# Optimization experiments

Hardware: AMD Instinct MI355X
Metric: run time of the kernel (lower is better)

## Reference

```python
import jax, jax.numpy as jnp
import numpy as np

FEA, DK, H = 512, 64, 8
B, L = 4, 2048
EPS = 1e-5


def _layernorm(x, g, b):
    mu = jnp.mean(x, axis=-1, keepdims=True)
    var = jnp.mean(jnp.square(x - mu), axis=-1, keepdims=True)
    return (x - mu) * jax.lax.rsqrt(var + EPS) * g + b


def setup_inputs() -> dict:
    key = jax.random.key(0)
    ks = jax.random.split(key, 12)
    d = {
        'qx': jax.random.normal(ks[0], (B, L, FEA), jnp.float32),
        'kx': jax.random.normal(ks[1], (B, L, FEA), jnp.float32),
        'vx': jax.random.normal(ks[2], (B, L, FEA), jnp.float32),
        'maskPAD': jax.random.randint(ks[3], (B, L, L), 0, 2, jnp.int32),
        # attention projections (stored as [in, out]); biases zero-init as in module
        'wq': jax.random.normal(ks[4], (FEA, DK * H), jnp.float32) * 0.02,
        'bq': jnp.zeros((DK * H,), jnp.float32),
        'wk': jax.random.normal(ks[5], (FEA, DK * H), jnp.float32) * 0.02,
        'bk': jnp.zeros((DK * H,), jnp.float32),
        'wv': jax.random.normal(ks[6], (FEA, DK * H), jnp.float32) * 0.02,
        'bv': jnp.zeros((DK * H,), jnp.float32),
        'wo': jax.random.normal(ks[7], (DK * H, FEA), jnp.float32) * 0.02,
        'bo': jnp.zeros((FEA,), jnp.float32),
        # FFN
        'w1': jax.random.normal(ks[8], (FEA, 4 * FEA), jnp.float32) * 0.02,
        'b1': jnp.zeros((4 * FEA,), jnp.float32),
        'w2': jax.random.normal(ks[9], (4 * FEA, FEA), jnp.float32) * 0.02,
        'b2': jnp.zeros((FEA,), jnp.float32),
        # layer norms
        'ln1_g': jnp.ones((FEA,), jnp.float32),
        'ln1_b': jnp.zeros((FEA,), jnp.float32),
        'ln2_g': jnp.ones((FEA,), jnp.float32),
        'ln2_b': jnp.zeros((FEA,), jnp.float32),
    }
    return d


def reference(qx, kx, vx, maskPAD, wq, bq, wk, bk, wv, bv, wo, bo,
              w1, b1, w2, b2, ln1_g, ln1_b, ln2_g, ln2_b):
    b, l, _ = qx.shape
    # project and split heads: [B, H, L, DK]
    q = (qx @ wq + bq).reshape(b, l, H, DK).transpose(0, 2, 1, 3)
    k = (kx @ wk + bk).reshape(b, l, H, DK).transpose(0, 2, 1, 3)
    v = (vx @ wv + bv).reshape(b, l, H, DK).transpose(0, 2, 1, 3)
    scores = jnp.einsum('bhqd,bhkd->bhqk', q, k) / np.sqrt(DK)  # [B,H,L,L]
    mask = (maskPAD == 0)[:, None, :, :]
    scores = jnp.where(mask, jnp.float32(-2 ** 15 + 1), scores)
    alpha = jax.nn.softmax(scores, axis=-1)
    z = jnp.einsum('bhqk,bhkd->bhqd', alpha, v)  # [B,H,L,DK]
    z = z.transpose(0, 2, 1, 3).reshape(b, l, H * DK)
    z = z @ wo + bo
    # post-LN FFN block (dropout = identity at inference)
    zn = _layernorm(vx + z, ln1_g, ln1_b)
    ffn = jax.nn.gelu(zn @ w1 + b1, approximate=False) @ w2 + b2
    return _layernorm(zn + ffn, ln2_g, ln2_b)
```

## Files before the change

### kernel.cpp

```cpp
#include <hip/hip_runtime.h>
#include <cstdint>


typedef __bf16 bf16;
typedef __bf16 bf16x8 __attribute__((ext_vector_type(8)));
typedef __bf16 bf16x2 __attribute__((ext_vector_type(2)));
typedef float floatx4 __attribute__((ext_vector_type(4)));
typedef unsigned uint2v __attribute__((ext_vector_type(2)));

__device__ __forceinline__ floatx4 mfma_bf16(bf16x8 a, bf16x8 b, floatx4 c) {
  return __builtin_amdgcn_mfma_f32_16x16x32_bf16(a, b, c, 0, 0, 0);
}

__device__ __forceinline__ void load_lds_16(const void* g, void* l) {
  auto gp = reinterpret_cast<const void __attribute__((address_space(1)))*>(
      reinterpret_cast<uintptr_t>(g));
  auto lp = reinterpret_cast<void __attribute__((address_space(3)))*>(
      (unsigned int)reinterpret_cast<uintptr_t>(l));
  __builtin_amdgcn_global_load_lds(gp, lp, 16, 0, 0);
}

__device__ __forceinline__ unsigned pack2(float a, float b) {
  bf16x2 p;
  p[0] = (bf16)a;
  p[1] = (bf16)b;
  return __builtin_bit_cast(unsigned, p);
}

__device__ __forceinline__ float gelu_f(float x) {
  float t = 0.7978845608f * (x + 0.044715f * x * x * x);
  float e = __builtin_amdgcn_exp2f(t * 2.885390082f);
  float th = 1.0f - 2.0f * __builtin_amdgcn_rcpf(e + 1.0f);
  return 0.5f * x * (1.0f + th);
}

#define PLANE128 2064
#define PLANE64 1040
#define KVCH 8320

__global__ void __launch_bounds__(256) prep_k(
    const float* __restrict__ wq, const float* __restrict__ wk,
    const float* __restrict__ wv, const float* __restrict__ wo,
    bf16* __restrict__ wqT, bf16* __restrict__ wkT, bf16* __restrict__ wvT,
    bf16* __restrict__ woT, const float* __restrict__ w1,
    bf16* __restrict__ w1T, const float* __restrict__ w2,
    bf16* __restrict__ w2T, const int* __restrict__ mpad,
    unsigned long long* __restrict__ mbits, const float* __restrict__ qx,
    const float* __restrict__ kx, const float* __restrict__ vx,
    bf16* __restrict__ xb) {
  __shared__ float tile[32][33];
  int bid = blockIdx.x, tid = threadIdx.x;
  int tx = tid & 31, ty = tid >> 5;
  if (bid < 3072) {
    const float* in;
    bf16* out;
    int m0, k0, K, M;
    if (bid < 1024) {
      int z = bid >> 8, r = bid & 255;
      in = (z == 0) ? wq : (z == 1) ? wk : (z == 2) ? wv : wo;
      out = (z == 0) ? wqT : (z == 1) ? wkT : (z == 2) ? wvT : woT;
      m0 = (r & 15) * 32; k0 = (r >> 4) * 32; K = 512; M = 512;
    } else if (bid < 2048) {
      int r = bid - 1024;
      in = w1; out = w1T;
      m0 = (r & 63) * 32; k0 = (r >> 6) * 32; K = 512; M = 2048;
    } else {
      int r = bid - 2048;
      in = w2; out = w2T;
      m0 = (r & 15) * 32; k0 = (r >> 4) * 32; K = 2048; M = 512;
    }
    for (int i = ty; i < 32; i += 8)
      tile[i][tx] = in[(size_t)(k0 + i) * M + m0 + tx];
    __syncthreads();
    for (int i = ty; i < 32; i += 8)
      out[(size_t)(m0 + i) * K + k0 + tx] = (bf16)tile[tx][i];
  } else if (bid < 5120) {
    int r = bid - 3072;
    int w0 = r * 128 + (tid >> 6) * 32;
    int lane = tid & 63;
#pragma unroll 4
    for (int i = 0; i < 32; ++i) {
      int w = w0 + i;
      int v = mpad[(size_t)w * 64 + lane];
      unsigned long long bmask = __ballot(v != 0);
      if (lane == 0) mbits[w] = bmask;
    }
  } else {
    int r = bid - 5120;
    size_t idx = ((size_t)r * 256 + tid) * 8;
    int sel = (int)(idx >> 22);
    size_t off = idx & ((1u << 22) - 1);
    const float* src = (sel == 0) ? qx : (sel == 1) ? kx : vx;
    float4 a = *(const float4*)(src + off);
    float4 b = *(const float4*)(src + off + 4);
    bf16x8 o;
    o[0] = (bf16)a.x; o[1] = (bf16)a.y; o[2] = (bf16)a.z; o[3] = (bf16)a.w;
    o[4] = (bf16)b.x; o[5] = (bf16)b.y; o[6] = (bf16)b.z; o[7] = (bf16)b.w;
    *(bf16x8*)(xb + idx) = o;
  }
}

template <int EPI>
__device__ __forceinline__ void epi_store(void* Cout, int n, int m, int M,
                                          float val) {
  if constexpr (EPI == 3) {
    ((bf16*)Cout)[(size_t)n * M + m] = (bf16)gelu_f(val);
  } else if constexpr (EPI == 4) {
    ((float*)Cout)[(size_t)n * M + m] = val;
  } else {
    ((float*)Cout)[(size_t)n * M + m] += val;
  }
}

template <int EPI, bool TALL>
__global__ void __launch_bounds__(256) gemm_bt(const bf16* __restrict__ A,
                                               const bf16* __restrict__ Bt,
                                               const float* __restrict__ bias,
                                               void* __restrict__ Cout,
                                               int M, int K, int lda, int ldb) {
  __shared__ __attribute__((aligned(16))) char As[8 * PLANE128];
  __shared__ __attribute__((aligned(16))) char Bs[TALL ? 8 * PLANE64 : 8 * PLANE128];
  int tid = threadIdx.x, wave = tid >> 6, lane = tid & 63;
  int lrow = lane & 15, quad = lane >> 4;
  int n0 = blockIdx.y * 128;
  int m0 = blockIdx.x * (TALL ? 64 : 128);
  int wr = wave >> 1, wc = wave & 1;
  floatx4 zero4 = {0.f, 0.f, 0.f, 0.f};
  constexpr int NI = TALL ? 2 : 4;
  floatx4 acc[NI][4];
#pragma unroll
  for (int i = 0; i < NI; ++i)
#pragma unroll
    for (int j = 0; j < 4; ++j) acc[i][j] = zero4;
  for (int k0 = 0; k0 < K; k0 += 64) {
    __syncthreads();
#pragma unroll
    for (int h = 0; h < 2; ++h) {
      int p = wave + 4 * h;
#pragma unroll
      for (int j = 0; j < 2; ++j) {
        int row = j * 64 + lane;
        load_lds_16(A + (size_t)(n0 + row) * lda + k0 + p * 8,
                    As + p * PLANE128 + j * 1024 + lane * 16);
      }
      if constexpr (TALL) {
        load_lds_16(Bt + (size_t)(m0 + lane) * ldb + k0 + p * 8,
                    Bs + p * PLANE64 + lane * 16);
      } else {
#pragma unroll
        for (int j = 0; j < 2; ++j) {
          int row = j * 64 + lane;
          load_lds_16(Bt + (size_t)(m0 + row) * ldb + k0 + p * 8,
                      Bs + p * PLANE128 + j * 1024 + lane * 16);
        }
      }
    }
    __syncthreads();
#pragma unroll
    for (int h = 0; h < 2; ++h) {
      int pb = h * 4 + quad;
      bf16x8 af[NI], bfr[4];
#pragma unroll
      for (int i = 0; i < NI; ++i) {
        int row = (TALL ? wave * 32 : wr * 64) + i * 16 + lrow;
        af[i] = *(const bf16x8*)(As + pb * PLANE128 + row * 16);
      }
#pragma unroll
      for (int j = 0; j < 4; ++j) {
        if constexpr (TALL)
          bfr[j] = *(const bf16x8*)(Bs + pb * PLANE64 + (j * 16 + lrow) * 16);
        else
          bfr[j] = *(const bf16x8*)(Bs + pb * PLANE128 +
                                    (wc * 64 + j * 16 + lrow) * 16);
      }
#pragma unroll
      for (int i = 0; i < NI; ++i)
#pragma unroll
        for (int j = 0; j < 4; ++j)
          acc[i][j] = mfma_bf16(af[i], bfr[j], acc[i][j]);
    }
  }
  float bv[4];
#pragma unroll
  for (int j = 0; j < 4; ++j) {
    int m = m0 + (TALL ? 0 : wc * 64) + j * 16 + lrow;
    bv[j] = (EPI == 5) ? 0.f : bias[m];
  }
#pragma unroll
  for (int i = 0; i < NI; ++i)
#pragma unroll
    for (int j = 0; j < 4; ++j)
#pragma unroll
      for (int r = 0; r < 4; ++r) {
        int n = n0 + (TALL ? wave * 32 : wr * 64) + i * 16 + quad * 4 + r;
        int m = m0 + (TALL ? 0 : wc * 64) + j * 16 + lrow;
        epi_store<EPI>(Cout, n, m, M, acc[i][j][r] + bv[j]);
      }
}

__global__ void __launch_bounds__(256) qkv_k(const bf16* __restrict__ xb,
                                             const bf16* __restrict__ wqT,
                                             const bf16* __restrict__ wkT,
                                             const bf16* __restrict__ wvT,
                                             const float* __restrict__ bq,
                                             const float* __restrict__ bk,
                                             const float* __restrict__ bv_,
                                             bf16* __restrict__ qh,
                                             bf16* __restrict__ kh,
                                             bf16* __restrict__ vt) {
  __shared__ __attribute__((aligned(16))) char As[8 * PLANE128];
  __shared__ __attribute__((aligned(16))) char Bs[8 * PLANE128];
  int tid = threadIdx.x, wave = tid >> 6, lane = tid & 63;
  int lrow = lane & 15, quad = lane >> 4;
  int seg = blockIdx.y >> 6;
  int n0 = (blockIdx.y & 63) * 128, m0 = blockIdx.x * 128;
  const bf16* Af = xb + ((size_t)seg << 22);
  const bf16* Bt = (seg == 0) ? wqT : (seg == 1) ? wkT : wvT;
  const float* bias = (seg == 0) ? bq : (seg == 1) ? bk : bv_;
  bf16* out = (seg == 0) ? qh : (seg == 1) ? kh : vt;
  int wr = wave >> 1, wc = wave & 1;
  floatx4 zero4 = {0.f, 0.f, 0.f, 0.f};
  floatx4 acc[4][4];
#pragma unroll
  for (int i = 0; i < 4; ++i)
#pragma unroll
    for (int j = 0; j < 4; ++j) acc[i][j] = zero4;
  for (int k0 = 0; k0 < 512; k0 += 64) {
    __syncthreads();
#pragma unroll
    for (int h = 0; h < 2; ++h) {
      int p = wave + 4 * h;
#pragma unroll
      for (int j = 0; j < 2; ++j) {
        int row = j * 64 + lane;
        load_lds_16(Af + (size_t)(n0 + row) * 512 + k0 + p * 8,
                    As + p * PLANE128 + j * 1024 + lane * 16);
        load_lds_16(Bt + (size_t)(m0 + row) * 512 + k0 + p * 8,
                    Bs + p * PLANE128 + j * 1024 + lane * 16);
      }
    }
    __syncthreads();
#pragma unroll
    for (int h = 0; h < 2; ++h) {
      int pb = h * 4 + quad;
      bf16x8 af[4], bfr[4];
#pragma unroll
      for (int t = 0; t < 4; ++t) {
        af[t] = *(const bf16x8*)(As + pb * PLANE128 + (wr * 64 + t * 16 + lrow) * 16);
        bfr[t] = *(const bf16x8*)(Bs + pb * PLANE128 + (wc * 64 + t * 16 + lrow) * 16);
      }
#pragma unroll
      for (int i = 0; i < 4; ++i)
#pragma unroll
        for (int j = 0; j < 4; ++j) acc[i][j] = mfma_bf16(af[i], bfr[j], acc[i][j]);
    }
  }
  float bvv[4];
#pragma unroll
  for (int j = 0; j < 4; ++j) bvv[j] = bias[m0 + wc * 64 + j * 16 + lrow];
  const float qscale = 0.1803368801f;
#pragma unroll
  for (int i = 0; i < 4; ++i)
#pragma unroll
    for (int j = 0; j < 4; ++j)
#pragma unroll
      for (int r = 0; r < 4; ++r) {
        int n = n0 + wr * 64 + i * 16 + quad * 4 + r;
        int m = m0 + wc * 64 + j * 16 + lrow;
        float val = acc[i][j][r] + bvv[j];
        int bb = n >> 11, l = n & 2047, hh = m >> 6, d = m & 63;
        if (seg == 0) {
          out[((size_t)((bb * 8 + hh) * 2048 + l)) * 64 + d] =
              (bf16)(val * qscale);
        } else {
          size_t tb_ = ((size_t)((bb * 8 + hh) * 32 + (l >> 6))) * 4096;
          if (seg == 1)
            out[tb_ + (d >> 3) * 512 + (l & 63) * 8 + (d & 7)] = (bf16)val;
          else
            out[tb_ + ((l >> 3) & 7) * 512 + d * 8 + (l & 7)] = (bf16)val;
        }
      }
}

__global__ void __launch_bounds__(512, 4) attn_k(const bf16* __restrict__ Qh,
                                                 const bf16* __restrict__ Kh,
                                                 const bf16* __restrict__ Vt,
                                                 const unsigned long long* __restrict__ MB,
                                                 bf16* __restrict__ Z) {
  __shared__ __attribute__((aligned(16))) char smem[8 * KVCH];
  int qt = blockIdx.x, h = blockIdx.y, b = blockIdx.z;
  int tid = threadIdx.x, wave = tid >> 6, lane = tid & 63;
  int hw = wave >> 2, wl = wave & 3;
  int lrow = lane & 15, quad = lane >> 4;
  int q0 = qt * 128;
  size_t headbase = (size_t)(b * 8 + h) * 2048 * 64;

  bf16x8 qf[2][2];
#pragma unroll
  for (int u = 0; u < 2; ++u) {
    const bf16* Qp =
        Qh + headbase + (size_t)(q0 + wl * 32 + u * 16 + lrow) * 64 + quad * 8;
    qf[u][0] = *(const bf16x8*)Qp;
    qf[u][1] = *(const bf16x8*)(Qp + 32);
  }

  floatx4 zero4 = {0.f, 0.f, 0.f, 0.f};
  floatx4 o_acc[2][4], acc_l[2];
#pragma unroll
  for (int u = 0; u < 2; ++u) {
    acc_l[u] = zero4;
#pragma unroll
    for (int dt = 0; dt < 4; ++dt) o_acc[u][dt] = zero4;
  }
  bf16x8 ones;
#pragma unroll
  for (int j = 0; j < 8; ++j) ones[j] = (bf16)1.0f;

  const bf16* Kt0 = Kh + headbase;
  const bf16* Vt0 = Vt + headbase;
  const uint2* MB0 =
      (const uint2*)(MB + ((size_t)b * 2048 + q0 + wl * 32 + lrow) * 32);
  int sh = quad * 4;

  char* KsH = smem + hw * 2 * KVCH;
  char* VsH = smem + 4 * KVCH + hw * 2 * KVCH;

  auto stage = [&](int buf, int kt) {
    const bf16* Ktile = Kt0 + (size_t)kt * 4096;
    const bf16* Vtile = Vt0 + (size_t)kt * 4096;
#pragma unroll
    for (int j = 0; j < 2; ++j) {
      int p = wl * 2 + j;
      load_lds_16(Ktile + p * 512 + lane * 8,
                  KsH + buf * KVCH + p * PLANE64 + lane * 16);
      load_lds_16(Vtile + p * 512 + lane * 8,
                  VsH + buf * KVCH + p * PLANE64 + lane * 16);
    }
  };

  int ktbase = hw * 16;
  stage(0, ktbase);
  uint2 mwc[2] = {MB0[ktbase], MB0[512 + ktbase]};

  for (int it = 0; it < 16; ++it) {
    int kt = ktbase + it;
    int cur = it & 1;
    __syncthreads();
    uint2 mwn[2];
    if (it < 15) {
      stage(cur ^ 1, kt + 1);
      mwn[0] = MB0[kt + 1];
      mwn[1] = MB0[512 + kt + 1];
    }
    const char* Kc = KsH + cur * KVCH;
    const char* Vc = VsH + cur * KVCH;
    unsigned S[2][4][2];
#pragma unroll
    for (int nt = 0; nt < 4; ++nt) {
      int R = nt * 16 + lrow;
      bf16x8 k0f = *(const bf16x8*)(Kc + quad * PLANE64 + R * 16);
      bf16x8 k1f = *(const bf16x8*)(Kc + (quad + 4) * PLANE64 + R * 16);
#pragma unroll
      for (int u = 0; u < 2; ++u) {
        floatx4 aa = zero4;
        aa = mfma_bf16(k0f, qf[u][0], aa);
        aa = mfma_bf16(k1f, qf[u][1], aa);
        unsigned wn = ((nt & 2) ? mwc[u].y : mwc[u].x) >> ((nt & 1) * 16 + sh);
        float e[4];
#pragma unroll
        for (int r = 0; r < 4; ++r)
          e[r] = (wn & (1u << r)) ? __builtin_amdgcn_exp2f(aa[r]) : 0.f;
        S[u][nt][0] = pack2(e[0], e[1]);
        S[u][nt][1] = pack2(e[2], e[3]);
      }
    }
    bf16x8 v0[4], v1[4];
#pragma unroll
    for (int dt = 0; dt < 4; ++dt) {
      int R = dt * 16 + lrow;
      v0[dt] = *(const bf16x8*)(Vc + quad * PLANE64 + R * 16);
      v1[dt] = *(const bf16x8*)(Vc + (quad + 4) * PLANE64 + R * 16);
    }
#pragma unroll
    for (int u = 0; u < 2; ++u) {
      union { unsigned w[4]; bf16x8 v; } pf[2];
#pragma unroll
      for (int half = 0; half < 2; ++half)
#pragma unroll
        for (int pr = 0; pr < 2; ++pr) {
          uint2v a = __builtin_amdgcn_permlane32_swap(
              S[u][half * 2][pr], S[u][half * 2 + 1][pr], false, false);
          uint2v c = __builtin_amdgcn_permlane16_swap(a[0], a[1], false, false);
          pf[half].w[pr] = c[0];
          pf[half].w[pr + 2] = c[1];
        }
      bf16x8 pf0 = pf[0].v, pf1 = pf[1].v;
      __builtin_amdgcn_s_setprio(1);
      acc_l[u] = mfma_bf16(pf0, ones, acc_l[u]);
      acc_l[u] = mfma_bf16(pf1, ones, acc_l[u]);
#pragma unroll
      for (int dt = 0; dt < 4; ++dt) {
        o_acc[u][dt] = mfma_bf16(pf0, v0[dt], o_acc[u][dt]);
        o_acc[u][dt] = mfma_bf16(pf1, v1[dt], o_acc[u][dt]);
      }
      __builtin_amdgcn_s_setprio(0);
    }
    if (it < 15) { mwc[0] = mwn[0]; mwc[1] = mwn[1]; }
  }

  __syncthreads();
  float* cb = (float*)smem;
  int cbase = (wl * 64 + lane) * 40;
  if (hw == 1) {
#pragma unroll
    for (int u = 0; u < 2; ++u) {
#pragma unroll
      for (int dt = 0; dt < 4; ++dt)
        *(floatx4*)(cb + cbase + (u * 4 + dt) * 4) = o_acc[u][dt];
      *(floatx4*)(cb + cbase + 32 + u * 4) = acc_l[u];
    }
  }
  __syncthreads();
  if (hw == 0) {
#pragma unroll
    for (int u = 0; u < 2; ++u) {
#pragma unroll
      for (int dt = 0; dt < 4; ++dt)
        o_acc[u][dt] += *(const floatx4*)(cb + cbase + (u * 4 + dt) * 4);
      acc_l[u] += *(const floatx4*)(cb + cbase + 32 + u * 4);
    }
#pragma unroll
    for (int u = 0; u < 2; ++u) {
      float lr[4];
#pragma unroll
      for (int r = 0; r < 4; ++r) lr[r] = 1.0f / acc_l[u][r];
#pragma unroll
      for (int dt = 0; dt < 4; ++dt)
#pragma unroll
        for (int r = 0; r < 4; ++r) {
          int qrow = q0 + wl * 32 + u * 16 + quad * 4 + r;
          int d = dt * 16 + lrow;
          Z[((size_t)(b * 2048 + qrow)) * 512 + h * 64 + d] =
              (bf16)(o_acc[u][dt][r] * lr[r]);
        }
    }
  }
}

template <bool A_BF16, bool OUT_BF16>
__global__ void __launch_bounds__(256) ln_k(const void* __restrict__ a_,
                                            const float* __restrict__ s,
                                            const float* __restrict__ g,
                                            const float* __restrict__ bta,
                                            void* __restrict__ out_) {
  int row = blockIdx.x * 4 + (threadIdx.x >> 6);
  int lane = threadIdx.x & 63;
  size_t base = (size_t)row * 512 + lane * 8;
  float x[8];
  float4 sa = *(const float4*)(s + base);
  float4 sb = *(const float4*)(s + base + 4);
  if constexpr (A_BF16) {
    bf16x8 av = *(const bf16x8*)((const bf16*)a_ + base);
    x[0] = (float)av[0] + sa.x; x[1] = (float)av[1] + sa.y;
    x[2] = (float)av[2] + sa.z; x[3] = (float)av[3] + sa.w;
    x[4] = (float)av[4] + sb.x; x[5] = (float)av[5] + sb.y;
    x[6] = (float)av[6] + sb.z; x[7] = (float)av[7] + sb.w;
  } else {
    float4 a0 = *(const float4*)((const float*)a_ + base);
    float4 a1 = *(const float4*)((const float*)a_ + base + 4);
    x[0] = a0.x + sa.x; x[1] = a0.y + sa.y; x[2] = a0.z + sa.z; x[3] = a0.w + sa.w;
    x[4] = a1.x + sb.x; x[5] = a1.y + sb.y; x[6] = a1.z + sb.z; x[7] = a1.w + sb.w;
  }
  float sum = 0.f;
#pragma unroll
  for (int i = 0; i < 8; ++i) sum += x[i];
#pragma unroll
  for (int off = 1; off < 64; off <<= 1) sum += __shfl_xor(sum, off, 64);
  float mu = sum * (1.0f / 512.0f);
  float vs = 0.f;
#pragma unroll
  for (int i = 0; i < 8; ++i) { float d = x[i] - mu; vs += d * d; }
#pragma unroll
  for (int off = 1; off < 64; off <<= 1) vs += __shfl_xor(vs, off, 64);
  float rstd = rsqrtf(vs * (1.0f / 512.0f) + 1e-5f);
  float4 g0 = *(const float4*)(g + lane * 8);
  float4 g1 = *(const float4*)(g + lane * 8 + 4);
  float4 b0 = *(const float4*)(bta + lane * 8);
  float4 b1 = *(const float4*)(bta + lane * 8 + 4);
  float gg[8] = {g0.x, g0.y, g0.z, g0.w, g1.x, g1.y, g1.z, g1.w};
  float bb[8] = {b0.x, b0.y, b0.z, b0.w, b1.x, b1.y, b1.z, b1.w};
  if constexpr (OUT_BF16) {
    bf16x8 o;
#pragma unroll
    for (int i = 0; i < 8; ++i)
      o[i] = (bf16)((x[i] - mu) * rstd * gg[i] + bb[i]);
    *(bf16x8*)((bf16*)out_ + base) = o;
  } else {
    float4 o0, o1;
    o0.x = (x[0] - mu) * rstd * gg[0] + bb[0];
    o0.y = (x[1] - mu) * rstd * gg[1] + bb[1];
    o0.z = (x[2] - mu) * rstd * gg[2] + bb[2];
    o0.w = (x[3] - mu) * rstd * gg[3] + bb[3];
    o1.x = (x[4] - mu) * rstd * gg[4] + bb[4];
    o1.y = (x[5] - mu) * rstd * gg[5] + bb[5];
    o1.z = (x[6] - mu) * rstd * gg[6] + bb[6];
    o1.w = (x[7] - mu) * rstd * gg[7] + bb[7];
    *(float4*)((float*)out_ + base) = o0;
    *(float4*)((float*)out_ + base + 4) = o1;
  }
}

extern "C" void kernel_launch(void* const* d_in, const int* in_sizes, int n_in,
                              void* d_out, int out_size, void* d_ws, size_t ws_size,
                              hipStream_t stream) {
  const float* qx = (const float*)d_in[0];
  const float* kx = (const float*)d_in[1];
  const float* vx = (const float*)d_in[2];
  const int* maskPAD = (const int*)d_in[3];
  const float* wq = (const float*)d_in[4];
  const float* bq = (const float*)d_in[5];
  const float* wk = (const float*)d_in[6];
  const float* bk = (const float*)d_in[7];
  const float* wv = (const float*)d_in[8];
  const float* bv = (const float*)d_in[9];
  const float* wo = (const float*)d_in[10];
  const float* bo = (const float*)d_in[11];
  const float* w1 = (const float*)d_in[12];
  const float* b1 = (const float*)d_in[13];
  const float* w2 = (const float*)d_in[14];
  const float* b2 = (const float*)d_in[15];
  const float* g1 = (const float*)d_in[16];
  const float* be1 = (const float*)d_in[17];
  const float* g2 = (const float*)d_in[18];
  const float* be2 = (const float*)d_in[19];

  char* w = (char*)d_ws;
  size_t off = 0;
  auto alloc = [&](size_t bytes) {
    void* p = w + off;
    off += (bytes + 255) & ~(size_t)255;
    return p;
  };
  bf16* wqT = (bf16*)alloc(512 * 512 * 2);
  bf16* wkT = (bf16*)alloc(512 * 512 * 2);
  bf16* wvT = (bf16*)alloc(512 * 512 * 2);
  bf16* woT = (bf16*)alloc(512 * 512 * 2);
  bf16* w1T = (bf16*)alloc(2048 * 512 * 2);
  bf16* w2T = (bf16*)alloc(512 * 2048 * 2);
  unsigned long long* mbits = (unsigned long long*)alloc((size_t)4 * 2048 * 32 * 8);
  bf16* xb = (bf16*)alloc((size_t)3 * 4194304 * 2);
  bf16* qh = (bf16*)alloc((size_t)8192 * 512 * 2);
  bf16* kh = (bf16*)alloc((size_t)8192 * 512 * 2);
  bf16* vt = (bf16*)alloc((size_t)8192 * 512 * 2);
  bf16* z = (bf16*)alloc((size_t)8192 * 512 * 2);
  float* s12 = (float*)qh;
  bf16* zn = vt;
  size_t h1_bytes = (size_t)8192 * 2048 * 2;
  bool big = (off + h1_bytes) <= ws_size;
  bf16* h1 = big ? (bf16*)alloc(h1_bytes) : z;

  prep_k<<<11264, 256, 0, stream>>>(wq, wk, wv, wo, wqT, wkT, wvT, woT, w1, w1T,
                                    w2, w2T, maskPAD, mbits, qx, kx, vx, xb);
  qkv_k<<<dim3(4, 192), 256, 0, stream>>>(xb, wqT, wkT, wvT, bq, bk, bv,
                                          qh, kh, vt);
  attn_k<<<dim3(16, 8, 4), 512, 0, stream>>>(qh, kh, vt, mbits, z);
  gemm_bt<4, true><<<dim3(8, 64), 256, 0, stream>>>(z, woT, bo, s12, 512, 512,
                                                    512, 512);
  ln_k<false, true><<<2048, 256, 0, stream>>>(vx, s12, g1, be1, zn);
  if (big) {
    gemm_bt<3, false><<<dim3(16, 64), 256, 0, stream>>>(zn, w1T, b1, h1, 2048,
                                                        512, 512, 512);
    gemm_bt<4, true><<<dim3(8, 64), 256, 0, stream>>>(h1, w2T, b2, s12, 512,
                                                      2048, 2048, 2048);
  } else {
    for (int p = 0; p < 4; ++p) {
      gemm_bt<3, true><<<dim3(8, 64), 256, 0, stream>>>(
          zn, w1T + (size_t)p * 512 * 512, b1 + p * 512, h1, 512, 512, 512, 512);
      if (p == 0)
        gemm_bt<4, true><<<dim3(8, 64), 256, 0, stream>>>(
            h1, w2T + p * 512, b2, s12, 512, 512, 512, 2048);
      else
        gemm_bt<5, true><<<dim3(8, 64), 256, 0, stream>>>(
            h1, w2T + p * 512, nullptr, s12, 512, 512, 512, 2048);
    }
  }
  ln_k<true, false><<<2048, 256, 0, stream>>>(zn, s12, g2, be2, (float*)d_out);
}
```

Baseline: 410.7 us.

## Double-buffer LDS tiles in GEMM and QKV kernels to overlap loads with MFMA

Splits the shared-memory A/B tiles into two buffers, each holding a K-slice of 32 instead of 64. The global-to-LDS copy for the next slice is issued before the MFMAs run on the current one, so each iteration needs one barrier instead of two. The aim is to hide global load latency behind matrix math in the projection, FFN and QKV GEMMs. In exchange there are twice as many loop iterations, each with less work per barrier. Whether the prefetch overlaps depends on the barrier's implicit memory wait, which could limit how much latency is hidden.

```diff
diff --git a/kernel.cpp b/kernel.cpp
--- a/kernel.cpp
+++ b/kernel.cpp
@@ -118,8 +118,9 @@
                                                const float* __restrict__ bias,
                                                void* __restrict__ Cout,
                                                int M, int K, int lda, int ldb) {
-  __shared__ __attribute__((aligned(16))) char As[8 * PLANE128];
-  __shared__ __attribute__((aligned(16))) char Bs[TALL ? 8 * PLANE64 : 8 * PLANE128];
+  __shared__ __attribute__((aligned(16))) char As[2][4 * PLANE128];
+  __shared__ __attribute__((aligned(16))) char Bs[2][TALL ? 4 * PLANE64
+                                                         : 4 * PLANE128];
   int tid = threadIdx.x, wave = tid >> 6, lane = tid & 63;
   int lrow = lane & 15, quad = lane >> 4;
   int n0 = blockIdx.y * 128;
@@ -132,53 +133,54 @@
   for (int i = 0; i < NI; ++i)
 #pragma unroll
     for (int j = 0; j < 4; ++j) acc[i][j] = zero4;
-  for (int k0 = 0; k0 < K; k0 += 64) {
-    __syncthreads();
-#pragma unroll
-    for (int h = 0; h < 2; ++h) {
-      int p = wave + 4 * h;
+
+  auto stage = [&](int buf, int k0) {
+    int p = wave;
+#pragma unroll
+    for (int j = 0; j < 2; ++j) {
+      int row = j * 64 + lane;
+      load_lds_16(A + (size_t)(n0 + row) * lda + k0 + p * 8,
+                  As[buf] + p * PLANE128 + j * 1024 + lane * 16);
+    }
+    if constexpr (TALL) {
+      load_lds_16(Bt + (size_t)(m0 + lane) * ldb + k0 + p * 8,
+                  Bs[buf] + p * PLANE64 + lane * 16);
+    } else {
 #pragma unroll
       for (int j = 0; j < 2; ++j) {
         int row = j * 64 + lane;
-        load_lds_16(A + (size_t)(n0 + row) * lda + k0 + p * 8,
-                    As + p * PLANE128 + j * 1024 + lane * 16);
+        load_lds_16(Bt + (size_t)(m0 + row) * ldb + k0 + p * 8,
+                    Bs[buf] + p * PLANE128 + j * 1024 + lane * 16);
       }
-      if constexpr (TALL) {
-        load_lds_16(Bt + (size_t)(m0 + lane) * ldb + k0 + p * 8,
-                    Bs + p * PLANE64 + lane * 16);
-      } else {
-#pragma unroll
-        for (int j = 0; j < 2; ++j) {
-          int row = j * 64 + lane;
-          load_lds_16(Bt + (size_t)(m0 + row) * ldb + k0 + p * 8,
-                      Bs + p * PLANE128 + j * 1024 + lane * 16);
-        }
-      }
-    }
+    }
+  };
+
+  stage(0, 0);
+  int nk = K >> 5;
+  for (int t = 0; t < nk; ++t) {
+    int cur = t & 1;
     __syncthreads();
-#pragma unroll
-    for (int h = 0; h < 2; ++h) {
-      int pb = h * 4 + quad;
-      bf16x8 af[NI], bfr[4];
-#pragma unroll
-      for (int i = 0; i < NI; ++i) {
-        int row = (TALL ? wave * 32 : wr * 64) + i * 16 + lrow;
-        af[i] = *(const bf16x8*)(As + pb * PLANE128 + row * 16);
-      }
-#pragma unroll
-      for (int j = 0; j < 4; ++j) {
-        if constexpr (TALL)
-          bfr[j] = *(const bf16x8*)(Bs + pb * PLANE64 + (j * 16 + lrow) * 16);
-        else
-          bfr[j] = *(const bf16x8*)(Bs + pb * PLANE128 +
-                                    (wc * 64 + j * 16 + lrow) * 16);
-      }
-#pragma unroll
-      for (int i = 0; i < NI; ++i)
-#pragma unroll
-        for (int j = 0; j < 4; ++j)
-          acc[i][j] = mfma_bf16(af[i], bfr[j], acc[i][j]);
-    }
+    if (t + 1 < nk) stage(cur ^ 1, (t + 1) * 32);
+    bf16x8 af[NI], bfr[4];
+#pragma unroll
+    for (int i = 0; i < NI; ++i) {
+      int row = (TALL ? wave * 32 : wr * 64) + i * 16 + lrow;
+      af[i] = *(const bf16x8*)(As[cur] + quad * PLANE128 + row * 16);
+    }
+#pragma unroll
+    for (int j = 0; j < 4; ++j) {
+      if constexpr (TALL)
+        bfr[j] = *(const bf16x8*)(Bs[cur] + quad * PLANE64 +
+                                  (j * 16 + lrow) * 16);
+      else
+        bfr[j] = *(const bf16x8*)(Bs[cur] + quad * PLANE128 +
+                                  (wc * 64 + j * 16 + lrow) * 16);
+    }
+#pragma unroll
+    for (int i = 0; i < NI; ++i)
+#pragma unroll
+      for (int j = 0; j < 4; ++j)
+        acc[i][j] = mfma_bf16(af[i], bfr[j], acc[i][j]);
   }
   float bv[4];
 #pragma unroll
@@ -208,8 +210,8 @@
                                              bf16* __restrict__ qh,
                                              bf16* __restrict__ kh,
                                              bf16* __restrict__ vt) {
-  __shared__ __attribute__((aligned(16))) char As[8 * PLANE128];
-  __shared__ __attribute__((aligned(16))) char Bs[8 * PLANE128];
+  __shared__ __attribute__((aligned(16))) char As[2][4 * PLANE128];
+  __shared__ __attribute__((aligned(16))) char Bs[2][4 * PLANE128];
   int tid = threadIdx.x, wave = tid >> 6, lane = tid & 63;
   int lrow = lane & 15, quad = lane >> 4;
   int seg = blockIdx.y >> 6;
@@ -225,35 +227,37 @@
   for (int i = 0; i < 4; ++i)
 #pragma unroll
     for (int j = 0; j < 4; ++j) acc[i][j] = zero4;
-  for (int k0 = 0; k0 < 512; k0 += 64) {
+
+  auto stage = [&](int buf, int k0) {
+    int p = wave;
+#pragma unroll
+    for (int j = 0; j < 2; ++j) {
+      int row = j * 64 + lane;
+      load_lds_16(Af + (size_t)(n0 + row) * 512 + k0 + p * 8,
+                  As[buf] + p * PLANE128 + j * 1024 + lane * 16);
+      load_lds_16(Bt + (size_t)(m0 + row) * 512 + k0 + p * 8,
+                  Bs[buf] + p * PLANE128 + j * 1024 + lane * 16);
+    }
+  };
+
+  stage(0, 0);
+  for (int t = 0; t < 16; ++t) {
+    int cur = t & 1;
     __syncthreads();
-#pragma unroll
-    for (int h = 0; h < 2; ++h) {
-      int p = wave + 4 * h;
-#pragma unroll
-      for (int j = 0; j < 2; ++j) {
-        int row = j * 64 + lane;
-        load_lds_16(Af + (size_t)(n0 + row) * 512 + k0 + p * 8,
-                    As + p * PLANE128 + j * 1024 + lane * 16);
-        load_lds_16(Bt + (size_t)(m0 + row) * 512 + k0 + p * 8,
-                    Bs + p * PLANE128 + j * 1024 + lane * 16);
-      }
-    }
-    __syncthreads();
-#pragma unroll
-    for (int h = 0; h < 2; ++h) {
-      int pb = h * 4 + quad;
-      bf16x8 af[4], bfr[4];
-#pragma unroll
-      for (int t = 0; t < 4; ++t) {
-        af[t] = *(const bf16x8*)(As + pb * PLANE128 + (wr * 64 + t * 16 + lrow) * 16);
-        bfr[t] = *(const bf16x8*)(Bs + pb * PLANE128 + (wc * 64 + t * 16 + lrow) * 16);
-      }
-#pragma unroll
-      for (int i = 0; i < 4; ++i)
-#pragma unroll
-        for (int j = 0; j < 4; ++j) acc[i][j] = mfma_bf16(af[i], bfr[j], acc[i][j]);
-    }
+    if (t < 15) stage(cur ^ 1, (t + 1) * 32);
+    bf16x8 af[4], bfr[4];
+#pragma unroll
+    for (int i = 0; i < 4; ++i)
+      af[i] = *(const bf16x8*)(As[cur] + quad * PLANE128 +
+                               (wr * 64 + i * 16 + lrow) * 16);
+#pragma unroll
+    for (int j = 0; j < 4; ++j)
+      bfr[j] = *(const bf16x8*)(Bs[cur] + quad * PLANE128 +
+                                (wc * 64 + j * 16 + lrow) * 16);
+#pragma unroll
+    for (int i = 0; i < 4; ++i)
+#pragma unroll
+      for (int j = 0; j < 4; ++j) acc[i][j] = mfma_bf16(af[i], bfr[j], acc[i][j]);
   }
   float bvv[4];
 #pragma unroll
```

Result: no change. 403.2 us (-1.8%).
